# Kernel optimization log

Hardware: AMD Instinct MI355X
Metric: run time of the kernel (lower is better)

The kernel has to match this reference:

```python
import jax, jax.numpy as jnp
import numpy as np

TOP_K = 2
SMOOTHING = 0.9


def setup_inputs() -> dict:
    key = jax.random.key(0)
    k1, k2, k3 = jax.random.split(key, 3)
    T, D, E = 16384, 2048, 64
    x = jax.random.normal(k1, (T, D), dtype=jnp.float32)
    gate_w = jax.random.normal(k2, (D, E), dtype=jnp.float32) * (1.0 / np.sqrt(D))
    expert_loads = jax.random.uniform(k3, (E,), dtype=jnp.float32)
    expert_loads = expert_loads / jnp.sum(expert_loads)  # normalized load estimate
    return {"x": x, "gate_w": gate_w, "expert_loads": expert_loads}


def reference(x, gate_w, expert_loads):
    T, _ = x.shape
    E = gate_w.shape[1]
    # Gate projection: [T, D] @ [D, E] -> [T, E]
    logits = jnp.matmul(x, gate_w)
    # Load-balancing bias injection (ExpertLoadBalancer.get_balancing_biases):
    # bias = -(load - 1/E) * 2, added to logits for expert *selection* only.
    biases = -(expert_loads - 1.0 / E) * 2.0
    _, top_idx = jax.lax.top_k(logits + biases[None, :], TOP_K)  # [T, K] int32
    # Routing weights: softmax over the selected (unbiased) logits.
    top_logits = jnp.take_along_axis(logits, top_idx, axis=1)  # [T, K]
    routing_weights = jax.nn.softmax(top_logits, axis=-1)  # [T, K]
    # Vectorized load update (replaces the Python double loop in update_loads):
    # scatter-add routing weights per expert, normalize by token count, EMA-smooth.
    current_loads = jax.ops.segment_sum(
        routing_weights.reshape(-1), top_idx.reshape(-1), num_segments=E
    ) / T
    new_loads = SMOOTHING * expert_loads + (1.0 - SMOOTHING) * current_loads
    return routing_weights, top_idx, new_loads
```

## Files before the change

kernel.cpp:

```cpp
#include <hip/hip_runtime.h>

#define TT 16384
#define DD 2048
#define EE 64

typedef __attribute__((ext_vector_type(8))) short bf16x8;
typedef __attribute__((ext_vector_type(8))) unsigned short ushort8;
typedef __attribute__((ext_vector_type(4))) float f32x4;

__device__ __forceinline__ unsigned short bf16_rne(float f) {
    unsigned u = __float_as_uint(f);
    return (unsigned short)((u + 0x7FFFu + ((u >> 16) & 1u)) >> 16);
}
__device__ __forceinline__ float bf16_f32(unsigned short h) {
    return __uint_as_float(((unsigned)h) << 16);
}

__device__ __forceinline__ void gload16(void* lds, const void* g) {
    __builtin_amdgcn_global_load_lds(
        (const __attribute__((address_space(1))) unsigned int*)g,
        (__attribute__((address_space(3))) unsigned int*)lds, 16, 0, 0);
}

__global__ __launch_bounds__(256)
void wconv(const float* __restrict__ wg, unsigned short* __restrict__ wpack) {
    const int t = (int)blockIdx.x * 256 + threadIdx.x;
    const int K0 = t >> 9, h = (t >> 8) & 1, m = (t >> 6) & 3, lane = t & 63;
    const int e = m * 16 + (lane & 15);
    const int ks = K0 * 32 + (lane >> 4) * 8;
    ushort8 v;
#pragma unroll
    for (int j = 0; j < 8; ++j) {
        const float f = wg[(size_t)(ks + j) * EE + e];
        const unsigned short hi = bf16_rne(f);
        v[j] = h ? bf16_rne(f - bf16_f32(hi)) : hi;
    }
    *(ushort8*)(wpack + ((size_t)(K0 * 8 + h * 4 + m) * 64 + lane) * 8) = v;
}

__global__ __launch_bounds__(512, 2)
void gate_fused(const float* __restrict__ x, const unsigned short* __restrict__ wpack,
                const float* __restrict__ loads, float* __restrict__ out,
                float* __restrict__ binpart) {
    __shared__ __align__(16) float arena[3 * 4096];
    __shared__ float bins[4][64];

    const int tid = threadIdx.x, lane = tid & 63, w = tid >> 6;
    const int tg = w >> 1, q = w & 1;
    const int tb = (int)blockIdx.x;

    f32x4 acc[4] = {{0,0,0,0},{0,0,0,0},{0,0,0,0},{0,0,0,0}};

    auto stage_x = [&](int s, float* rb) {
#pragma unroll
        for (int i = 0; i < 2; ++i) {
            const int n = (w << 1) | i;
            const int qh = n >> 3, g = n & 7;
            const int r = (g << 3) + (lane >> 3);
            const int c = (lane & 7) ^ ((lane >> 3) & 7);
            gload16(rb + qh * 2048 + g * 256,
                    x + (size_t)(tb * 64 + r) * DD + qh * 1024 + s * 32 + c * 4);
        }
    };
    auto loadW = [&](int t, bf16x8 (&wh)[4], bf16x8 (&wl)[4]) {
        const unsigned short* base = wpack + (size_t)((q << 5) + t) * 4096 + lane * 8;
#pragma unroll
        for (int m = 0; m < 4; ++m) {
            wh[m] = *(const bf16x8*)(base + (size_t)m * 512);
            wl[m] = *(const bf16x8*)(base + (size_t)(4 + m) * 512);
        }
    };
    auto compute = [&](const float* xq, bf16x8 (&wh)[4], bf16x8 (&wl)[4]) {
        const int col = lane & 15;
        const int row = (tg << 4) + col;
        const int kgc = (lane >> 4) << 1;
        const int sw = row & 7;
        const f32x4 va = *(const f32x4*)(xq + ((row << 3) + (kgc ^ sw)) * 4);
        const f32x4 vb = *(const f32x4*)(xq + ((row << 3) + ((kgc + 1) ^ sw)) * 4);
        const float cf[8] = {va.x, va.y, va.z, va.w, vb.x, vb.y, vb.z, vb.w};
        bf16x8 bhi, blo;
#pragma unroll
        for (int j = 0; j < 8; ++j) {
            const unsigned short h = bf16_rne(cf[j]);
            bhi[j] = (short)h;
            blo[j] = (short)bf16_rne(cf[j] - bf16_f32(h));
        }
#pragma unroll
        for (int m = 0; m < 4; ++m) {
            acc[m] = __builtin_amdgcn_mfma_f32_16x16x32_bf16(wh[m], bhi, acc[m], 0, 0, 0);
            acc[m] = __builtin_amdgcn_mfma_f32_16x16x32_bf16(wh[m], blo, acc[m], 0, 0, 0);
            acc[m] = __builtin_amdgcn_mfma_f32_16x16x32_bf16(wl[m], bhi, acc[m], 0, 0, 0);
        }
    };

    float *p0 = arena, *p1 = arena + 4096, *p2 = arena + 8192;
    bf16x8 whA[4], wlA[4], whB[4], wlB[4];

    stage_x(0, p0);
    stage_x(1, p1);
    loadW(0, whA, wlA);
    asm volatile("s_waitcnt vmcnt(10)" ::: "memory");
    __builtin_amdgcn_s_barrier();

    for (int s = 0; s < 30; s += 2) {
        stage_x(s + 2, p2);
        loadW(s + 1, whB, wlB);
        compute(p0 + (q << 11), whA, wlA);
        asm volatile("s_waitcnt vmcnt(10)" ::: "memory");
        __builtin_amdgcn_s_barrier();
        { float* t_ = p0; p0 = p1; p1 = p2; p2 = t_; }

        stage_x(s + 3, p2);
        loadW(s + 2, whA, wlA);
        compute(p0 + (q << 11), whB, wlB);
        asm volatile("s_waitcnt vmcnt(10)" ::: "memory");
        __builtin_amdgcn_s_barrier();
        { float* t_ = p0; p0 = p1; p1 = p2; p2 = t_; }
    }
    loadW(31, whB, wlB);
    compute(p0 + (q << 11), whA, wlA);
    asm volatile("s_waitcnt vmcnt(8)" ::: "memory");
    __builtin_amdgcn_s_barrier();
    compute(p1 + (q << 11), whB, wlB);

    float* accb = arena;
    if (q == 1) {
#pragma unroll
        for (int m = 0; m < 4; ++m)
            *(f32x4*)(accb + ((size_t)(tg * 64 + lane) * 16 + m * 4)) = acc[m];
    }
    __syncthreads();
    if (q != 0) return;

    f32x4 r[4];
#pragma unroll
    for (int m = 0; m < 4; ++m) {
        const f32x4 t_ = *(const f32x4*)(accb + ((size_t)(tg * 64 + lane) * 16 + m * 4));
        r[m].x = acc[m].x + t_.x; r[m].y = acc[m].y + t_.y;
        r[m].z = acc[m].z + t_.z; r[m].w = acc[m].w + t_.w;
    }

    const int col = lane & 15;
    const int tok = tb * 64 + tg * 16 + col;
    const int erow = (lane >> 4) * 4;
    float v1 = -3.4e38f, u1 = 0.0f, v2 = -3.4e38f, u2 = 0.0f;
    int i1 = 0x7fffffff, i2 = 0x7fffffff;
#pragma unroll
    for (int m = 0; m < 4; ++m)
#pragma unroll
        for (int rr = 0; rr < 4; ++rr) {
            const int e = m * 16 + erow + rr;
            const float u = r[m][rr];
            const float b = u - (loads[e] - 0.015625f) * 2.0f;
            if ((b > v1) || (b == v1 && e < i1)) {
                v2 = v1; u2 = u1; i2 = i1;
                v1 = b;  u1 = u;  i1 = e;
            } else if ((b > v2) || (b == v2 && e < i2)) {
                v2 = b; u2 = u; i2 = e;
            }
        }
#pragma unroll
    for (int s = 0; s < 2; ++s) {
        const int mask = 16 << s;
        const float ov1 = __shfl_xor(v1, mask), ou1 = __shfl_xor(u1, mask);
        const float ov2 = __shfl_xor(v2, mask), ou2 = __shfl_xor(u2, mask);
        const int oi1 = __shfl_xor(i1, mask), oi2 = __shfl_xor(i2, mask);
        if ((ov1 > v1) || (ov1 == v1 && oi1 < i1)) {
            if ((v1 > ov2) || (v1 == ov2 && i1 < oi2)) { v2 = v1; u2 = u1; i2 = i1; }
            else                                        { v2 = ov2; u2 = ou2; i2 = oi2; }
            v1 = ov1; u1 = ou1; i1 = oi1;
        } else if ((ov1 > v2) || (ov1 == v2 && oi1 < i2)) {
            v2 = ov1; u2 = ou1; i2 = oi1;
        }
    }

    bins[tg][lane] = 0.0f;
    if (lane < 16) {
        const float mx = fmaxf(u1, u2);
        const float e1 = __expf(u1 - mx), e2 = __expf(u2 - mx);
        const float w1 = e1 / (e1 + e2), w2 = e2 / (e1 + e2);
        *(float2*)(out + 2 * tok) = make_float2(w1, w2);
        *(float2*)(out + 2 * TT + 2 * tok) = make_float2((float)i1, (float)i2);
        atomicAdd(&bins[tg][i1], w1);
        atomicAdd(&bins[tg][i2], w2);
    }
    binpart[(size_t)(tb * 4 + tg) * 64 + lane] = bins[tg][lane];
}

__global__ __launch_bounds__(256)
void finalize1(const float* __restrict__ binpart, float* __restrict__ binmid) {
    __shared__ float p[4][64];
    const int e = threadIdx.x & 63, sub = threadIdx.x >> 6;
    float s = 0.0f;
#pragma unroll 4
    for (int r = 0; r < 16; ++r)
        s += binpart[(size_t)(((int)blockIdx.x * 4 + sub) * 16 + r) * 64 + e];
    p[sub][e] = s;
    __syncthreads();
    if (sub == 0)
        binmid[(int)blockIdx.x * 64 + e] = ((p[0][e] + p[1][e]) + p[2][e]) + p[3][e];
}

__global__ __launch_bounds__(64)
void finalize2(const float* __restrict__ binmid, const float* __restrict__ loads,
               float* __restrict__ out) {
    const int e = threadIdx.x;
    float s = 0.0f;
#pragma unroll
    for (int j = 0; j < 16; ++j) s += binmid[j * 64 + e];
    out[4 * TT + e] = 0.9f * loads[e] + 0.1f * (s * (1.0f / 16384.0f));
}

extern "C" void kernel_launch(void* const* d_in, const int* in_sizes, int n_in,
                              void* d_out, int out_size, void* d_ws, size_t ws_size,
                              hipStream_t stream) {
    const float* x = (const float*)d_in[0];
    const float* wg = (const float*)d_in[1];
    const float* loads = (const float*)d_in[2];
    float* out = (float*)d_out;

    unsigned short* wpack = (unsigned short*)d_ws;
    float* binpart = (float*)(wpack + (size_t)64 * 8 * 64 * 8);
    float* binmid = binpart + 1024 * 64;

    hipLaunchKernelGGL(wconv, dim3(128), dim3(256), 0, stream, wg, wpack);
    hipLaunchKernelGGL(gate_fused, dim3(256), dim3(512), 0, stream,
                       x, wpack, loads, out, binpart);
    hipLaunchKernelGGL(finalize1, dim3(16), dim3(256), 0, stream, binpart, binmid);
    hipLaunchKernelGGL(finalize2, dim3(1), dim3(64), 0, stream, binmid, loads, out);
}
```

Before: 48.91 us.

## Halve tokens per block, split K four ways, use packed bf16 convert

Each block now handles 32 tokens instead of 64, and the 8 waves split the K dimension four ways instead of two. This doubles the grid to 512 blocks, which gives better CU coverage on the 256-CU part, and raises the launch-bounds occupancy hint. The hi/lo bf16 split now uses the hardware v_cvt_pk_bf16_f32 instruction instead of manual rounding. The cost is a three-way cross-wave reduction through LDS (with padded stride) plus an extra barrier. The binpart layout changes to 2 groups per block, and finalize1 keeps indexing 1024 rows, which is consistent with 512 blocks x 2 groups.

```diff
diff --git a/kernel.cpp b/kernel.cpp
--- a/kernel.cpp
+++ b/kernel.cpp
@@ -15,7 +15,16 @@
 __device__ __forceinline__ float bf16_f32(unsigned short h) {
     return __uint_as_float(((unsigned)h) << 16);
 }
-
+__device__ __forceinline__ unsigned cvt_pk(float lo, float hi) {
+    unsigned r;
+    asm("v_cvt_pk_bf16_f32 %0, %1, %2" : "=v"(r) : "v"(lo), "v"(hi));
+    return r;
+}
+__device__ __forceinline__ bf16x8 pack4(unsigned a, unsigned b, unsigned c, unsigned d) {
+    union { unsigned u[4]; bf16x8 v; } t;
+    t.u[0] = a; t.u[1] = b; t.u[2] = c; t.u[3] = d;
+    return t.v;
+}
 __device__ __forceinline__ void gload16(void* lds, const void* g) {
     __builtin_amdgcn_global_load_lds(
         (const __attribute__((address_space(1))) unsigned int*)g,
@@ -38,15 +47,15 @@
     *(ushort8*)(wpack + ((size_t)(K0 * 8 + h * 4 + m) * 64 + lane) * 8) = v;
 }
 
-__global__ __launch_bounds__(512, 2)
+__global__ __launch_bounds__(512, 4)
 void gate_fused(const float* __restrict__ x, const unsigned short* __restrict__ wpack,
                 const float* __restrict__ loads, float* __restrict__ out,
                 float* __restrict__ binpart) {
     __shared__ __align__(16) float arena[3 * 4096];
-    __shared__ float bins[4][64];
+    __shared__ float bins[2][64];
 
     const int tid = threadIdx.x, lane = tid & 63, w = tid >> 6;
-    const int tg = w >> 1, q = w & 1;
+    const int tg = w >> 2, q = w & 3;
     const int tb = (int)blockIdx.x;
 
     f32x4 acc[4] = {{0,0,0,0},{0,0,0,0},{0,0,0,0},{0,0,0,0}};
@@ -55,36 +64,40 @@
 #pragma unroll
         for (int i = 0; i < 2; ++i) {
             const int n = (w << 1) | i;
-            const int qh = n >> 3, g = n & 7;
-            const int r = (g << 3) + (lane >> 3);
-            const int c = (lane & 7) ^ ((lane >> 3) & 7);
-            gload16(rb + qh * 2048 + g * 256,
-                    x + (size_t)(tb * 64 + r) * DD + qh * 1024 + s * 32 + c * 4);
+            const int qw = n >> 2, g = n & 3;
+            const int rowp = lane >> 3;
+            const int row = g * 8 + rowp;
+            const int c = (lane & 7) ^ rowp;
+            gload16(rb + qw * 1024 + g * 256,
+                    x + (size_t)(tb * 32 + row) * DD + qw * 512 + s * 32 + c * 4);
         }
     };
     auto loadW = [&](int t, bf16x8 (&wh)[4], bf16x8 (&wl)[4]) {
-        const unsigned short* base = wpack + (size_t)((q << 5) + t) * 4096 + lane * 8;
+        const unsigned short* base = wpack + (size_t)(q * 16 + t) * 4096 + lane * 8;
 #pragma unroll
         for (int m = 0; m < 4; ++m) {
             wh[m] = *(const bf16x8*)(base + (size_t)m * 512);
             wl[m] = *(const bf16x8*)(base + (size_t)(4 + m) * 512);
         }
     };
-    auto compute = [&](const float* xq, bf16x8 (&wh)[4], bf16x8 (&wl)[4]) {
-        const int col = lane & 15;
-        const int row = (tg << 4) + col;
+    auto compute = [&](const float* rb, bf16x8 (&wh)[4], bf16x8 (&wl)[4]) {
+        const float* xq = rb + q * 1024;
+        const int row = tg * 16 + (lane & 15);
         const int kgc = (lane >> 4) << 1;
         const int sw = row & 7;
-        const f32x4 va = *(const f32x4*)(xq + ((row << 3) + (kgc ^ sw)) * 4);
-        const f32x4 vb = *(const f32x4*)(xq + ((row << 3) + ((kgc + 1) ^ sw)) * 4);
+        const f32x4 va = *(const f32x4*)(xq + row * 32 + ((kgc) ^ sw) * 4);
+        const f32x4 vb = *(const f32x4*)(xq + row * 32 + ((kgc + 1) ^ sw) * 4);
         const float cf[8] = {va.x, va.y, va.z, va.w, vb.x, vb.y, vb.z, vb.w};
-        bf16x8 bhi, blo;
-#pragma unroll
-        for (int j = 0; j < 8; ++j) {
-            const unsigned short h = bf16_rne(cf[j]);
-            bhi[j] = (short)h;
-            blo[j] = (short)bf16_rne(cf[j] - bf16_f32(h));
-        }
+        unsigned ph[4], pl[4];
+#pragma unroll
+        for (int j = 0; j < 4; ++j) {
+            ph[j] = cvt_pk(cf[2 * j], cf[2 * j + 1]);
+            const float h0 = __uint_as_float(ph[j] << 16);
+            const float h1 = __uint_as_float(ph[j] & 0xFFFF0000u);
+            pl[j] = cvt_pk(cf[2 * j] - h0, cf[2 * j + 1] - h1);
+        }
+        const bf16x8 bhi = pack4(ph[0], ph[1], ph[2], ph[3]);
+        const bf16x8 blo = pack4(pl[0], pl[1], pl[2], pl[3]);
 #pragma unroll
         for (int m = 0; m < 4; ++m) {
             acc[m] = __builtin_amdgcn_mfma_f32_16x16x32_bf16(wh[m], bhi, acc[m], 0, 0, 0);
@@ -102,32 +115,34 @@
     asm volatile("s_waitcnt vmcnt(10)" ::: "memory");
     __builtin_amdgcn_s_barrier();
 
-    for (int s = 0; s < 30; s += 2) {
+#pragma unroll 1
+    for (int s = 0; s < 14; s += 2) {
         stage_x(s + 2, p2);
         loadW(s + 1, whB, wlB);
-        compute(p0 + (q << 11), whA, wlA);
+        compute(p0, whA, wlA);
         asm volatile("s_waitcnt vmcnt(10)" ::: "memory");
         __builtin_amdgcn_s_barrier();
         { float* t_ = p0; p0 = p1; p1 = p2; p2 = t_; }
 
         stage_x(s + 3, p2);
         loadW(s + 2, whA, wlA);
-        compute(p0 + (q << 11), whB, wlB);
+        compute(p0, whB, wlB);
         asm volatile("s_waitcnt vmcnt(10)" ::: "memory");
         __builtin_amdgcn_s_barrier();
         { float* t_ = p0; p0 = p1; p1 = p2; p2 = t_; }
     }
-    loadW(31, whB, wlB);
-    compute(p0 + (q << 11), whA, wlA);
+    loadW(15, whB, wlB);
+    compute(p0, whA, wlA);
     asm volatile("s_waitcnt vmcnt(8)" ::: "memory");
     __builtin_amdgcn_s_barrier();
-    compute(p1 + (q << 11), whB, wlB);
-
+    compute(p1, whB, wlB);
+
+    __syncthreads();
     float* accb = arena;
-    if (q == 1) {
+    if (q != 0) {
 #pragma unroll
         for (int m = 0; m < 4; ++m)
-            *(f32x4*)(accb + ((size_t)(tg * 64 + lane) * 16 + m * 4)) = acc[m];
+            *(f32x4*)(accb + ((size_t)((q - 1) * 128 + tg * 64 + lane) * 20 + m * 4)) = acc[m];
     }
     __syncthreads();
     if (q != 0) return;
@@ -135,13 +150,18 @@
     f32x4 r[4];
 #pragma unroll
     for (int m = 0; m < 4; ++m) {
-        const f32x4 t_ = *(const f32x4*)(accb + ((size_t)(tg * 64 + lane) * 16 + m * 4));
-        r[m].x = acc[m].x + t_.x; r[m].y = acc[m].y + t_.y;
-        r[m].z = acc[m].z + t_.z; r[m].w = acc[m].w + t_.w;
+        f32x4 s_ = acc[m];
+#pragma unroll
+        for (int qq = 0; qq < 3; ++qq) {
+            const f32x4 t_ =
+                *(const f32x4*)(accb + ((size_t)(qq * 128 + tg * 64 + lane) * 20 + m * 4));
+            s_.x += t_.x; s_.y += t_.y; s_.z += t_.z; s_.w += t_.w;
+        }
+        r[m] = s_;
     }
 
     const int col = lane & 15;
-    const int tok = tb * 64 + tg * 16 + col;
+    const int tok = tb * 32 + tg * 16 + col;
     const int erow = (lane >> 4) * 4;
     float v1 = -3.4e38f, u1 = 0.0f, v2 = -3.4e38f, u2 = 0.0f;
     int i1 = 0x7fffffff, i2 = 0x7fffffff;
@@ -184,7 +204,7 @@
         atomicAdd(&bins[tg][i1], w1);
         atomicAdd(&bins[tg][i2], w2);
     }
-    binpart[(size_t)(tb * 4 + tg) * 64 + lane] = bins[tg][lane];
+    binpart[(size_t)(tb * 2 + tg) * 64 + lane] = bins[tg][lane];
 }
 
 __global__ __launch_bounds__(256)
@@ -224,7 +244,7 @@
     float* binmid = binpart + 1024 * 64;
 
     hipLaunchKernelGGL(wconv, dim3(128), dim3(256), 0, stream, wg, wpack);
-    hipLaunchKernelGGL(gate_fused, dim3(256), dim3(512), 0, stream,
+    hipLaunchKernelGGL(gate_fused, dim3(512), dim3(512), 0, stream,
                        x, wpack, loads, out, binpart);
     hipLaunchKernelGGL(finalize1, dim3(16), dim3(256), 0, stream, binpart, binmid);
     hipLaunchKernelGGL(finalize2, dim3(1), dim3(64), 0, stream, binmid, loads, out);
```

Result: faster. 45.48 us (-7.0%).
